# Kernel tuning notes

Hardware: AMD Instinct MI355X
Metric: run time of the kernel (lower is better)

The kernel has to match this reference:

```python
import jax, jax.numpy as jnp
import numpy as np

B, A, C = 1, 196416, 90
H = W = 1024
SCORE_THRESHOLD = 0.05
MAX_DETECTIONS = 100
# RetinaNet-style BBoxTransform normalization (mean=0, std=[0.1,0.1,0.2,0.2])
STD = (0.1, 0.1, 0.2, 0.2)


def setup_inputs() -> dict:
    key = jax.random.key(0)
    k1, k2, k3, k4, k5, k6, k7 = jax.random.split(key, 7)
    x = jax.random.normal(k1, (B, 3, H, W), dtype=jnp.float32)
    regression = jax.random.normal(k2, (B, A, 4), dtype=jnp.float32) * 0.1
    classification = jax.random.normal(k3, (B, A, C), dtype=jnp.float32)
    # valid anchor boxes (x1, y1, x2, y2)
    cx = jax.random.uniform(k4, (B, A), minval=0.0, maxval=float(W))
    cy = jax.random.uniform(k5, (B, A), minval=0.0, maxval=float(H))
    aw = jax.random.uniform(k6, (B, A), minval=16.0, maxval=256.0)
    ah = jax.random.uniform(k7, (B, A), minval=16.0, maxval=256.0)
    anchors = jnp.stack([cx - 0.5 * aw, cy - 0.5 * ah, cx + 0.5 * aw, cy + 0.5 * ah], axis=2).astype(jnp.float32)
    return {"x": x, "regression": regression, "classification": classification, "anchors": anchors}


def _decode_clip(anchors, regression, img_h, img_w):
    # BBoxTransform: deltas (dx, dy, dw, dh) scaled by std, applied to anchor center/size
    wa = anchors[..., 2] - anchors[..., 0]
    ha = anchors[..., 3] - anchors[..., 1]
    cxa = anchors[..., 0] + 0.5 * wa
    cya = anchors[..., 1] + 0.5 * ha
    dx = regression[..., 0] * STD[0]
    dy = regression[..., 1] * STD[1]
    dw = regression[..., 2] * STD[2]
    dh = regression[..., 3] * STD[3]
    cx = cxa + dx * wa
    cy = cya + dy * ha
    w = jnp.exp(dw) * wa
    h = jnp.exp(dh) * ha
    # ClipBoxes: x1,y1 clamped at 0; x2,y2 clamped at image width/height
    x1 = jnp.maximum(cx - 0.5 * w, 0.0)
    y1 = jnp.maximum(cy - 0.5 * h, 0.0)
    x2 = jnp.minimum(cx + 0.5 * w, float(img_w))
    y2 = jnp.minimum(cy + 0.5 * h, float(img_h))
    return jnp.stack([x1, y1, x2, y2], axis=2)  # [B, A, 4]


def reference(x, regression, classification, anchors):
    img_h, img_w = x.shape[2], x.shape[3]
    boxes = _decode_clip(anchors, regression, img_h, img_w)  # [1, A, 4]
    probs = jax.nn.sigmoid(classification)                    # [1, A, C]
    scores = jnp.max(probs, axis=2)                           # [1, A]
    classes = jnp.argmax(probs, axis=2)                       # [1, A]
    valid_scores = jnp.where(scores > SCORE_THRESHOLD, scores, 0.0)
    vb = boxes[0]            # [A, 4]
    vc = classes[0]          # [A]
    vs = valid_scores[0]     # [A]
    k = min(MAX_DETECTIONS, vs.shape[0])
    _, top_idx = jax.lax.top_k(vs, k)
    final_boxes = vb[top_idx]
    final_scores = vs[top_idx]
    final_classes = vc[top_idx]
    return (final_boxes, final_scores, final_classes)
```

## Files before the change

kernel.cpp:

```cpp
#include <hip/hip_runtime.h>
#include <cmath>

#define A_CNT 196416
#define C_CNT 90
#define QUADS (A_CNT / 4)
#define QITERS (QUADS / 8)
#define TOPK 100u
#define CAPB 2048
#define NB_RED 512
#define NWAVES 2048
#define NB_GAT 192

#define OFF_HIST1 785664u
#define OFF_CTRL  789760u
#define OFF_CANDA 789824u
#define OFF_CANDB 790336u

#define AGENT_LD(p)    __hip_atomic_load((p), __ATOMIC_RELAXED, __HIP_MEMORY_SCOPE_AGENT)
#define AGENT_ST(p, v) __hip_atomic_store((p), (v), __ATOMIC_RELAXED, __HIP_MEMORY_SCOPE_AGENT)


#define LOADQ(V, qq)                                                        \
    {                                                                       \
        const float4* __restrict__ r4_ = cls4 + (size_t)(qq) * 90;          \
        _Pragma("unroll")                                                   \
        for (int i_ = 0; i_ < 12; ++i_) {                                   \
            const int j_ = s + 8 * i_;                                      \
            V[i_] = r4_[(j_ < 90) ? j_ : 89];   \
        }                                                                   \
    }                                                                       \
    __builtin_amdgcn_sched_barrier(0);

#define REDUCE_EMIT(V, qq)                                                  \
    {                                                                       \
        float m0 = -INFINITY, m1 = -INFINITY, m2 = -INFINITY, m3 = -INFINITY; \
        _Pragma("unroll")                                                   \
        for (int i_ = 0; i_ < 12; ++i_) {                                   \
            const int j_ = s + 8 * i_;                                      \
            const float4 vv = V[i_];                                        \
            const float a01 = fmaxf(vv.x, vv.y), a23 = fmaxf(vv.z, vv.w);   \
            const float all = fmaxf(a01, a23);                              \
            if (j_ < 22)       m0 = fmaxf(m0, all);                         \
            else if (j_ == 22) { m0 = fmaxf(m0, a01); m1 = fmaxf(m1, a23); }\
            else if (j_ < 45)  m1 = fmaxf(m1, all);                         \
            else if (j_ < 67)  m2 = fmaxf(m2, all);                         \
            else if (j_ == 67) { m2 = fmaxf(m2, a01); m3 = fmaxf(m3, a23); }\
            else if (j_ < 90)  m3 = fmaxf(m3, all);                         \
        }                                                                   \
        _Pragma("unroll")                                                   \
        for (int d_ = 1; d_ < 8; d_ <<= 1) {                                \
            m0 = fmaxf(m0, __shfl_xor(m0, d_));                             \
            m1 = fmaxf(m1, __shfl_xor(m1, d_));                             \
            m2 = fmaxf(m2, __shfl_xor(m2, d_));                             \
            m3 = fmaxf(m3, __shfl_xor(m3, d_));                             \
        }                                                                   \
        if (s == 0) {                                                       \
            float p0 = 1.0f / (1.0f + expf(-m0));    \
            float p1 = 1.0f / (1.0f + expf(-m1));                           \
            float p2 = 1.0f / (1.0f + expf(-m2));                           \
            float p3 = 1.0f / (1.0f + expf(-m3));                           \
            unsigned k0 = (p0 > 0.05f) ? __float_as_uint(p0) : 0u;          \
            unsigned k1 = (p1 > 0.05f) ? __float_as_uint(p1) : 0u;          \
            unsigned k2 = (p2 > 0.05f) ? __float_as_uint(p2) : 0u;          \
            unsigned k3 = (p3 > 0.05f) ? __float_as_uint(p3) : 0u;          \
            *(uint4*)(keys + 4 * (size_t)(qq)) = make_uint4(k0, k1, k2, k3);\
            unsigned h0 = k0 ? (min(k0 >> 16, 0x3F80u) - 0x3D4Bu) : 0u;     \
            unsigned h1 = k1 ? (min(k1 >> 16, 0x3F80u) - 0x3D4Bu) : 0u;     \
            unsigned h2 = k2 ? (min(k2 >> 16, 0x3F80u) - 0x3D4Bu) : 0u;     \
            unsigned h3 = k3 ? (min(k3 >> 16, 0x3F80u) - 0x3D4Bu) : 0u;     \
            atomicAdd(&lhist[h0], 1u);                                      \
            atomicAdd(&lhist[h1], 1u);                                      \
            atomicAdd(&lhist[h2], 1u);                                      \
            atomicAdd(&lhist[h3], 1u);                                      \
        }                                                                   \
    }

#define SUFFIX_SCAN_SDATA()                                                 \
    for (int d_ = 1; d_ < 256; d_ <<= 1) {                                  \
        __syncthreads();                                                    \
        unsigned add_ = (t + d_ < 256) ? sdata[t + d_] : 0u;                \
        __syncthreads();                                                    \
        sdata[t] += add_;                                                   \
    }                                                                       \
    __syncthreads();

__global__ __launch_bounds__(256, 2) void k_reduce(const float* __restrict__ cls,
                                                   unsigned* __restrict__ keys,
                                                   unsigned* __restrict__ hist1,
                                                   unsigned* __restrict__ ctrl) {
    __shared__ unsigned lhist[576];
    __shared__ unsigned sdata[256];
    __shared__ unsigned sbin[2];
    __shared__ int sflag;
    const int t = threadIdx.x;
    for (int j = t; j < 576; j += 256) lhist[j] = 0u;
    __syncthreads();

    const int lane = t & 63;
    const int g = lane >> 3, s = lane & 7;
    const int w = blockIdx.x * 4 + (t >> 6);
    const float4* __restrict__ cls4 = (const float4*)cls;

    const int qi2 = w + 2 * NWAVES;
    const bool has2 = (qi2 < QITERS);
    const int q0 = w * 8 + g;
    const int q1 = (w + NWAVES) * 8 + g;
    const int q2 = (has2 ? qi2 : w) * 8 + g;

    float4 vA[12], vB[12], vC[12];
    LOADQ(vA, q0);
    LOADQ(vB, q1);
    LOADQ(vC, q2);
    REDUCE_EMIT(vA, q0);
    REDUCE_EMIT(vB, q1);
    if (has2) REDUCE_EMIT(vC, q2);

    __syncthreads();
    for (int j = t; j < 576; j += 256) {
        unsigned c = lhist[j];
        if (c) atomicAdd(&hist1[j], c);
    }
    __syncthreads();
    if (t == 0) sflag = (atomicAdd(&ctrl[8], 1u) == NB_RED - 1u) ? 1 : 0;
    __syncthreads();
    if (!sflag) return;

    unsigned ssum = 0;
#pragma unroll
    for (int j = 0; j < 4; ++j) ssum += AGENT_LD(&hist1[t * 4 + j]);
    sdata[t] = ssum;
    SUFFIX_SCAN_SDATA()
    {
        unsigned mysuf  = sdata[t];
        unsigned nxtsuf = (t < 255) ? sdata[t + 1] : 0u;
        if (nxtsuf < TOPK && mysuf >= TOPK) { sbin[0] = (unsigned)t; sbin[1] = nxtsuf; }
    }
    __syncthreads();
    const unsigned chunkB = sbin[0];
    const unsigned gAbove = sbin[1];
    sdata[t] = (t < 4) ? AGENT_LD(&hist1[chunkB * 4 + t]) : 0u;
    SUFFIX_SCAN_SDATA()
    {
        unsigned mysuf  = sdata[t] + gAbove;
        unsigned nxtsuf = ((t < 255) ? sdata[t + 1] : 0u) + gAbove;
        if (nxtsuf < TOPK && mysuf >= TOPK) {
            unsigned bin = chunkB * 4 + (unsigned)t;
            ctrl[0] = bin ? (bin + 0x3D4Bu) : 0u;
            ctrl[1] = nxtsuf;
        }
    }
}

__global__ __launch_bounds__(256) void k_gather(const float* __restrict__ cls,
                                                const float* __restrict__ reg,
                                                const float* __restrict__ anc,
                                                const unsigned* __restrict__ keys,
                                                unsigned* __restrict__ ctrl,
                                                unsigned* __restrict__ candA,
                                                unsigned* __restrict__ candB,
                                                float* __restrict__ out) {
    __shared__ unsigned sAi[128], sAk[128];
    __shared__ unsigned sBi[CAPB], sBk[CAPB];
    __shared__ unsigned sdata[256];
    __shared__ unsigned sbin[2];
    __shared__ unsigned sel[TOPK], selk[TOPK];
    __shared__ int sflag;
    const int t = threadIdx.x;

    const unsigned binB = ctrl[0];
    const int i4 = blockIdx.x * 256 + t;
    if (i4 < A_CNT / 4) {
        uint4 k = ((const uint4*)keys)[i4];
        const unsigned base = (unsigned)(4 * i4);
#pragma unroll
        for (int j = 0; j < 4; ++j) {
            unsigned kk = (j == 0) ? k.x : (j == 1) ? k.y : (j == 2) ? k.z : k.w;
            unsigned t16 = kk >> 16;
            if (t16 > binB) {
                unsigned q = atomicAdd(&ctrl[5], 1u);
                if (q < 128u) AGENT_ST(&candA[q], base + j);
            } else if (t16 == binB) {
                unsigned q = atomicAdd(&ctrl[6], 1u);
                if (q < (unsigned)CAPB) AGENT_ST(&candB[q], base + j);
            }
        }
    }
    __syncthreads();
    if (t == 0) sflag = (atomicAdd(&ctrl[9], 1u) == (unsigned)NB_GAT - 1u) ? 1 : 0;
    __syncthreads();
    if (!sflag) return;

    const unsigned nA = min(AGENT_LD(&ctrl[5]), 128u);
    const unsigned nB = min(AGENT_LD(&ctrl[6]), (unsigned)CAPB);
    const unsigned need = TOPK - nA;

    if (t < (int)nA) { unsigned i = AGENT_LD(&candA[t]); sAi[t] = i; sAk[t] = keys[i]; }
    for (unsigned e = (unsigned)t; e < nB; e += 256u) {
        unsigned i = AGENT_LD(&candB[e]); sBi[e] = i; sBk[e] = keys[i];
    }
    sdata[t] = 0u;
    __syncthreads();
    for (unsigned e = (unsigned)t; e < nB; e += 256u)
        atomicAdd(&sdata[(sBk[e] >> 8) & 0xFFu], 1u);
    SUFFIX_SCAN_SDATA()
    {
        unsigned mysuf  = sdata[t];
        unsigned nxtsuf = (t < 255) ? sdata[t + 1] : 0u;
        if (nxtsuf < need && mysuf >= need) { sbin[0] = (unsigned)t; sbin[1] = nxtsuf; }
    }
    __syncthreads();
    const unsigned bstar = sbin[0];
    const unsigned S1    = sbin[1];

    if (t < (int)nA) {
        unsigned mi = sAi[t], mk = sAk[t], r = 0;
        for (unsigned j = 0; j < nA; ++j) {
            unsigned ok = sAk[j];
            if (ok > mk || (ok == mk && sAi[j] < mi)) r++;
        }
        sel[r] = mi; selk[r] = mk;
    }
    for (unsigned e = (unsigned)t; e < nB; e += 256u) {
        unsigned mk = sBk[e], mi = sBi[e];
        unsigned mb = (mk >> 8) & 0xFFu;
        if (mb > bstar) {
            unsigned r = 0;
            for (unsigned j = 0; j < nB; ++j) {
                unsigned ok = sBk[j];
                if (((ok >> 8) & 0xFFu) > bstar &&
                    (ok > mk || (ok == mk && sBi[j] < mi))) r++;
            }
            sel[nA + r] = mi; selk[nA + r] = mk;
        } else if (mb == bstar) {
            unsigned r = 0;
            for (unsigned j = 0; j < nB; ++j) {
                unsigned ok = sBk[j];
                if (((ok >> 8) & 0xFFu) == bstar &&
                    (ok > mk || (ok == mk && sBi[j] < mi))) r++;
            }
            if (r < need - S1) { sel[nA + S1 + r] = mi; selk[nA + S1 + r] = mk; }
        }
    }
    __syncthreads();

    if (t < (int)TOPK) {
        const unsigned a = sel[t];
        const float2* __restrict__ row = (const float2*)(cls + (size_t)a * C_CNT);
        float2 vr[45];
#pragma unroll
        for (int c = 0; c < 45; ++c) vr[c] = row[c];
        float bv = -INFINITY; int bi = 0;
#pragma unroll
        for (int c = 0; c < 45; ++c) {
            if (vr[c].x > bv) { bv = vr[c].x; bi = 2 * c; }
            if (vr[c].y > bv) { bv = vr[c].y; bi = 2 * c + 1; }
        }
        float score = __uint_as_float(selk[t]);
        const float4 an = ((const float4*)anc)[a];
        const float4 rg = ((const float4*)reg)[a];
        float wa = an.z - an.x, ha = an.w - an.y;
        float cxa = an.x + 0.5f * wa, cya = an.y + 0.5f * ha;
        float dx = rg.x * 0.1f, dy = rg.y * 0.1f;
        float dw = rg.z * 0.2f, dh = rg.w * 0.2f;
        float cx = cxa + dx * wa, cy = cya + dy * ha;
        float w2 = expf(dw) * wa, h2 = expf(dh) * ha;
        out[t * 4 + 0] = fmaxf(cx - 0.5f * w2, 0.0f);
        out[t * 4 + 1] = fmaxf(cy - 0.5f * h2, 0.0f);
        out[t * 4 + 2] = fminf(cx + 0.5f * w2, 1024.0f);
        out[t * 4 + 3] = fminf(cy + 0.5f * h2, 1024.0f);
        out[400 + t] = score;
        out[500 + t] = (float)bi;
    }
}

extern "C" void kernel_launch(void* const* d_in, const int* in_sizes, int n_in,
                              void* d_out, int out_size, void* d_ws, size_t ws_size,
                              hipStream_t stream) {
    const float* reg = (const float*)d_in[1];
    const float* cls = (const float*)d_in[2];
    const float* anc = (const float*)d_in[3];
    float* out = (float*)d_out;
    char* ws = (char*)d_ws;
    unsigned* keys  = (unsigned*)ws;
    unsigned* hist1 = (unsigned*)(ws + OFF_HIST1);
    unsigned* ctrl  = (unsigned*)(ws + OFF_CTRL);
    unsigned* candA = (unsigned*)(ws + OFF_CANDA);
    unsigned* candB = (unsigned*)(ws + OFF_CANDB);

    hipMemsetAsync(hist1, 0, 4096 + 64, stream);
    k_reduce<<<NB_RED, 256, 0, stream>>>(cls, keys, hist1, ctrl);
    k_gather<<<NB_GAT, 256, 0, stream>>>(cls, reg, anc, keys, ctrl, candA, candB, out);
}
```

Before: 155.6 us.

## Stage class rows through LDS with async global_load_lds double buffering

The reduction kernel now streams classification rows with global_load_lds straight into per-wave LDS double buffers and overlaps loads with the max reduction using explicit vmcnt waits. Each wave handles 8 anchors per 2880-byte chunk, with 16 lanes per anchor pair, instead of holding 12 float4 registers per lane across three batches. The grid grows from 512 to 1280 blocks. The gather kernel drops the selk array and rereads the score from keys. This aims to raise memory-level parallelism and cut register pressure, at the cost of hand-written waitcnt asm and more LDS use.

```diff
diff --git a/kernel.cpp b/kernel.cpp
--- a/kernel.cpp
+++ b/kernel.cpp
@@ -3,12 +3,12 @@
 
 #define A_CNT 196416
 #define C_CNT 90
-#define QUADS (A_CNT / 4)
-#define QITERS (QUADS / 8)
+#define CLS_BYTES (196416u * 90u * 4u)
+#define NWI2 (A_CNT / 8)
 #define TOPK 100u
 #define CAPB 2048
-#define NB_RED 512
-#define NWAVES 2048
+#define NB_RED 1280
+#define NWAVES 5120
 #define NB_GAT 192
 
 #define OFF_HIST1 785664u
@@ -20,58 +20,57 @@
 #define AGENT_ST(p, v) __hip_atomic_store((p), (v), __ATOMIC_RELAXED, __HIP_MEMORY_SCOPE_AGENT)
 
 
-#define LOADQ(V, qq)                                                        \
+typedef __attribute__((address_space(1))) const void* gas_t;
+typedef __attribute__((address_space(3))) void* las_t;
+
+#define STAGE(B, wi)                                                        \
     {                                                                       \
-        const float4* __restrict__ r4_ = cls4 + (size_t)(qq) * 90;          \
-        _Pragma("unroll")                                                   \
-        for (int i_ = 0; i_ < 12; ++i_) {                                   \
-            const int j_ = s + 8 * i_;                                      \
-            V[i_] = r4_[(j_ < 90) ? j_ : 89];   \
-        }                                                                   \
+        asm volatile("s_waitcnt lgkmcnt(0)" ::: "memory");                  \
+        const char* gb_ = clsb + (size_t)(wi) * 2880 + lane * 16;           \
+        const char* g2_ = gb_ + 2048;                                       \
+        if (g2_ > clsend16) g2_ = clsend16;     \
+        __builtin_amdgcn_global_load_lds((gas_t)gb_,          (las_t)(B),          16, 0, 0); \
+        __builtin_amdgcn_global_load_lds((gas_t)(gb_ + 1024), (las_t)((B) + 1024), 16, 0, 0); \
+        __builtin_amdgcn_global_load_lds((gas_t)g2_,          (las_t)((B) + 2048), 16, 0, 0); \
     }                                                                       \
     __builtin_amdgcn_sched_barrier(0);
 
-#define REDUCE_EMIT(V, qq)                                                  \
+#define WAITV(N)                                                            \
+    asm volatile("s_waitcnt vmcnt(" #N ")" ::: "memory");                   \
+    __builtin_amdgcn_sched_barrier(0);
+
+#define FMAX4(v) fmaxf(fmaxf((v).x, (v).y), fmaxf((v).z, (v).w))
+
+#define REDUCE_EMIT(B, wi)                                                  \
     {                                                                       \
-        float m0 = -INFINITY, m1 = -INFINITY, m2 = -INFINITY, m3 = -INFINITY; \
+        const float4* q_ = (const float4*)((B) + g * 720);                  \
+        const float4 v0_ = q_[s];                                           \
+        const float4 v1_ = q_[s + 16];                                      \
+        const float4 v2_ = q_[(s < 13) ? (s + 32) : s];                     \
+        float m0 = FMAX4(v0_);                        \
+        float m1 = -INFINITY;                                               \
+        {                                                                   \
+            const float a01 = fmaxf(v1_.x, v1_.y), a23 = fmaxf(v1_.z, v1_.w); \
+            if (s < 6)       m0 = fmaxf(m0, fmaxf(a01, a23));               \
+            else if (s == 6) { m0 = fmaxf(m0, a01); m1 = a23; }             \
+            else             m1 = fmaxf(a01, a23);                          \
+        }                                                                   \
+        if (s < 13) m1 = fmaxf(m1, FMAX4(v2_));           \
         _Pragma("unroll")                                                   \
-        for (int i_ = 0; i_ < 12; ++i_) {                                   \
-            const int j_ = s + 8 * i_;                                      \
-            const float4 vv = V[i_];                                        \
-            const float a01 = fmaxf(vv.x, vv.y), a23 = fmaxf(vv.z, vv.w);   \
-            const float all = fmaxf(a01, a23);                              \
-            if (j_ < 22)       m0 = fmaxf(m0, all);                         \
-            else if (j_ == 22) { m0 = fmaxf(m0, a01); m1 = fmaxf(m1, a23); }\
-            else if (j_ < 45)  m1 = fmaxf(m1, all);                         \
-            else if (j_ < 67)  m2 = fmaxf(m2, all);                         \
-            else if (j_ == 67) { m2 = fmaxf(m2, a01); m3 = fmaxf(m3, a23); }\
-            else if (j_ < 90)  m3 = fmaxf(m3, all);                         \
-        }                                                                   \
-        _Pragma("unroll")                                                   \
-        for (int d_ = 1; d_ < 8; d_ <<= 1) {                                \
+        for (int d_ = 1; d_ < 16; d_ <<= 1) {                               \
             m0 = fmaxf(m0, __shfl_xor(m0, d_));                             \
             m1 = fmaxf(m1, __shfl_xor(m1, d_));                             \
-            m2 = fmaxf(m2, __shfl_xor(m2, d_));                             \
-            m3 = fmaxf(m3, __shfl_xor(m3, d_));                             \
         }                                                                   \
         if (s == 0) {                                                       \
             float p0 = 1.0f / (1.0f + expf(-m0));    \
             float p1 = 1.0f / (1.0f + expf(-m1));                           \
-            float p2 = 1.0f / (1.0f + expf(-m2));                           \
-            float p3 = 1.0f / (1.0f + expf(-m3));                           \
             unsigned k0 = (p0 > 0.05f) ? __float_as_uint(p0) : 0u;          \
             unsigned k1 = (p1 > 0.05f) ? __float_as_uint(p1) : 0u;          \
-            unsigned k2 = (p2 > 0.05f) ? __float_as_uint(p2) : 0u;          \
-            unsigned k3 = (p3 > 0.05f) ? __float_as_uint(p3) : 0u;          \
-            *(uint4*)(keys + 4 * (size_t)(qq)) = make_uint4(k0, k1, k2, k3);\
+            *(uint2*)(keys + 2 * ((size_t)(wi) * 4 + g)) = make_uint2(k0, k1); \
             unsigned h0 = k0 ? (min(k0 >> 16, 0x3F80u) - 0x3D4Bu) : 0u;     \
             unsigned h1 = k1 ? (min(k1 >> 16, 0x3F80u) - 0x3D4Bu) : 0u;     \
-            unsigned h2 = k2 ? (min(k2 >> 16, 0x3F80u) - 0x3D4Bu) : 0u;     \
-            unsigned h3 = k3 ? (min(k3 >> 16, 0x3F80u) - 0x3D4Bu) : 0u;     \
             atomicAdd(&lhist[h0], 1u);                                      \
             atomicAdd(&lhist[h1], 1u);                                      \
-            atomicAdd(&lhist[h2], 1u);                                      \
-            atomicAdd(&lhist[h3], 1u);                                      \
         }                                                                   \
     }
 
@@ -84,10 +83,11 @@
     }                                                                       \
     __syncthreads();
 
-__global__ __launch_bounds__(256, 2) void k_reduce(const float* __restrict__ cls,
-                                                   unsigned* __restrict__ keys,
-                                                   unsigned* __restrict__ hist1,
-                                                   unsigned* __restrict__ ctrl) {
+__global__ __launch_bounds__(256) void k_reduce(const float* __restrict__ cls,
+                                                unsigned* __restrict__ keys,
+                                                unsigned* __restrict__ hist1,
+                                                unsigned* __restrict__ ctrl) {
+    __shared__ __align__(16) char stg[4][2][3072];
     __shared__ unsigned lhist[576];
     __shared__ unsigned sdata[256];
     __shared__ unsigned sbin[2];
@@ -97,23 +97,37 @@
     __syncthreads();
 
     const int lane = t & 63;
-    const int g = lane >> 3, s = lane & 7;
-    const int w = blockIdx.x * 4 + (t >> 6);
-    const float4* __restrict__ cls4 = (const float4*)cls;
-
-    const int qi2 = w + 2 * NWAVES;
-    const bool has2 = (qi2 < QITERS);
-    const int q0 = w * 8 + g;
-    const int q1 = (w + NWAVES) * 8 + g;
-    const int q2 = (has2 ? qi2 : w) * 8 + g;
-
-    float4 vA[12], vB[12], vC[12];
-    LOADQ(vA, q0);
-    LOADQ(vB, q1);
-    LOADQ(vC, q2);
-    REDUCE_EMIT(vA, q0);
-    REDUCE_EMIT(vB, q1);
-    if (has2) REDUCE_EMIT(vC, q2);
+    const int g = lane >> 4, s = lane & 15;
+    const int wv = t >> 6;
+    const int w = blockIdx.x * 4 + wv;
+    const char* clsb = (const char*)cls;
+    const char* clsend16 = clsb + (CLS_BYTES - 16u);
+    char* b0 = &stg[wv][0][0];
+    char* b1 = &stg[wv][1][0];
+
+    const int wi0 = w;
+    const int wi1 = w + NWAVES;
+    const int wi2 = w + 2 * NWAVES;
+    const int wi3 = w + 3 * NWAVES;
+    const int wi4 = w + 4 * NWAVES;
+    const bool has4 = (wi4 < NWI2);
+    const int wi4c = has4 ? wi4 : wi0;
+
+    STAGE(b0, wi0);
+    STAGE(b1, wi1);
+    WAITV(3)
+    REDUCE_EMIT(b0, wi0);
+    STAGE(b0, wi2);
+    WAITV(4)
+    REDUCE_EMIT(b1, wi1);
+    STAGE(b1, wi3);
+    WAITV(4)
+    REDUCE_EMIT(b0, wi2);
+    STAGE(b0, wi4c);
+    WAITV(4)
+    REDUCE_EMIT(b1, wi3);
+    WAITV(1)
+    if (has4) REDUCE_EMIT(b0, wi4);
 
     __syncthreads();
     for (int j = t; j < 576; j += 256) {
@@ -125,6 +139,7 @@
     __syncthreads();
     if (!sflag) return;
 
+    const unsigned target = TOPK;
     unsigned ssum = 0;
 #pragma unroll
     for (int j = 0; j < 4; ++j) ssum += AGENT_LD(&hist1[t * 4 + j]);
@@ -133,7 +148,7 @@
     {
         unsigned mysuf  = sdata[t];
         unsigned nxtsuf = (t < 255) ? sdata[t + 1] : 0u;
-        if (nxtsuf < TOPK && mysuf >= TOPK) { sbin[0] = (unsigned)t; sbin[1] = nxtsuf; }
+        if (nxtsuf < target && mysuf >= target) { sbin[0] = (unsigned)t; sbin[1] = nxtsuf; }
     }
     __syncthreads();
     const unsigned chunkB = sbin[0];
@@ -143,7 +158,7 @@
     {
         unsigned mysuf  = sdata[t] + gAbove;
         unsigned nxtsuf = ((t < 255) ? sdata[t + 1] : 0u) + gAbove;
-        if (nxtsuf < TOPK && mysuf >= TOPK) {
+        if (nxtsuf < target && mysuf >= target) {
             unsigned bin = chunkB * 4 + (unsigned)t;
             ctrl[0] = bin ? (bin + 0x3D4Bu) : 0u;
             ctrl[1] = nxtsuf;
@@ -163,7 +178,7 @@
     __shared__ unsigned sBi[CAPB], sBk[CAPB];
     __shared__ unsigned sdata[256];
     __shared__ unsigned sbin[2];
-    __shared__ unsigned sel[TOPK], selk[TOPK];
+    __shared__ unsigned sel[TOPK];
     __shared__ int sflag;
     const int t = threadIdx.x;
 
@@ -218,7 +233,7 @@
             unsigned ok = sAk[j];
             if (ok > mk || (ok == mk && sAi[j] < mi)) r++;
         }
-        sel[r] = mi; selk[r] = mk;
+        sel[r] = mi;
     }
     for (unsigned e = (unsigned)t; e < nB; e += 256u) {
         unsigned mk = sBk[e], mi = sBi[e];
@@ -230,7 +245,7 @@
                 if (((ok >> 8) & 0xFFu) > bstar &&
                     (ok > mk || (ok == mk && sBi[j] < mi))) r++;
             }
-            sel[nA + r] = mi; selk[nA + r] = mk;
+            sel[nA + r] = mi;
         } else if (mb == bstar) {
             unsigned r = 0;
             for (unsigned j = 0; j < nB; ++j) {
@@ -238,7 +253,7 @@
                 if (((ok >> 8) & 0xFFu) == bstar &&
                     (ok > mk || (ok == mk && sBi[j] < mi))) r++;
             }
-            if (r < need - S1) { sel[nA + S1 + r] = mi; selk[nA + S1 + r] = mk; }
+            if (r < need - S1) sel[nA + S1 + r] = mi;
         }
     }
     __syncthreads();
@@ -255,7 +270,7 @@
             if (vr[c].x > bv) { bv = vr[c].x; bi = 2 * c; }
             if (vr[c].y > bv) { bv = vr[c].y; bi = 2 * c + 1; }
         }
-        float score = __uint_as_float(selk[t]);
+        float score = __uint_as_float(keys[a]);
         const float4 an = ((const float4*)anc)[a];
         const float4 rg = ((const float4*)reg)[a];
         float wa = an.z - an.x, ha = an.w - an.y;
```

Measured after the change: 165.0 us. 6.0% more time.
